# Kernel tuning notes

Hardware: AMD Instinct MI355X
Metric: run time of the kernel (lower is better)

## Reference

```python
import jax, jax.numpy as jnp
import numpy as np

IDIM = 1024
ODIM = 1024
NHEADS = 16
B, S = 4, 1024


def setup_inputs() -> dict:
    key = jax.random.key(0)
    k1, k2, k3, k4, k5, k6 = jax.random.split(key, 6)
    m_feats = jax.random.normal(k1, (B, S, IDIM), dtype=jnp.float32)
    mask = jax.random.randint(k2, (B, S), 0, 2, dtype=jnp.int32)
    # torch Linear weights stored pre-transposed: y = x @ W + b
    W_c = jax.random.normal(k3, (IDIM, 2 * ODIM), dtype=jnp.float32) * 0.02
    b_c = jnp.zeros((2 * ODIM,), dtype=jnp.float32)
    W_v = jax.random.normal(k4, (IDIM, ODIM), dtype=jnp.float32) * 0.02
    b_v = jnp.zeros((ODIM,), dtype=jnp.float32)
    return {"m_feats": m_feats, "mask": mask, "W_c": W_c, "b_c": b_c, "W_v": W_v, "b_v": b_v}


def reference(m_feats, mask, W_c, b_c, W_v, b_v):
    # dp = 0.0 -> dropout is identity (eval-mode equivalence)
    Bn, Sn, _ = m_feats.shape
    odim = W_v.shape[1]
    dh = odim // NHEADS
    m_k = m_feats @ W_v + b_v            # v_lin  -> keys   [B,S,odim]
    m_trans = m_feats @ W_c + b_c        # c_lin  -> [B,S,2*odim]
    m_q = m_trans[..., :odim]            # queries
    m_v = m_trans[..., odim:]            # values
    mk = m_k.reshape(Bn, Sn, NHEADS, dh)
    mq = m_q.reshape(Bn, Sn, NHEADS, dh)
    mv = m_v.reshape(Bn, Sn, NHEADS, dh)
    # original: scores = K @ Q^T / sqrt(dh); softmax over the Q (last) axis
    scores = jnp.einsum('bihd,bjhd->bhij', mk, mq) / jnp.sqrt(jnp.float32(dh))
    maskf = mask.astype(jnp.float32)
    scores = jnp.where(maskf[:, None, None, :] == 0.0, jnp.float32(-1e9), scores)
    w = jax.nn.softmax(scores, axis=-1)               # [B,H,S,S]
    r = jnp.einsum('bhij,bjhd->bihd', w, mv).reshape(Bn, Sn, odim)
    updated_m = m_feats + r
    return updated_m, w
```

## Files before the change

kernel.cpp:

```cpp
#include <hip/hip_runtime.h>
#include <cstddef>

typedef short short8 __attribute__((ext_vector_type(8)));
typedef float f32x4 __attribute__((ext_vector_type(4)));

#define SS 1024
#define NH 16
#define DH 64
#define NB 4

static __device__ __forceinline__ unsigned short f2bf(float f) {
    union { float f; unsigned int i; } x; x.f = f;
    unsigned int r = x.i + 0x7FFFu + ((x.i >> 16) & 1u);
    return (unsigned short)(r >> 16);
}
static __device__ __forceinline__ float bf2f(unsigned short u) {
    union { unsigned int i; float f; } x; x.i = ((unsigned int)u) << 16;
    return x.f;
}

static __device__ __forceinline__ void g2l16(const void* g, void* l) {
    __builtin_amdgcn_global_load_lds(
        (const __attribute__((address_space(1))) unsigned int*)g,
        (__attribute__((address_space(3))) unsigned int*)l, 16, 0, 0);
}

__global__ __launch_bounds__(256) void cast_mf(const float* __restrict__ in,
                                               unsigned short* __restrict__ out) {
    size_t i = ((size_t)blockIdx.x * 256 + threadIdx.x) * 4;
    float4 v = *(const float4*)(in + i);
    short4 o;
    o.x = (short)f2bf(v.x); o.y = (short)f2bf(v.y);
    o.z = (short)f2bf(v.z); o.w = (short)f2bf(v.w);
    *(short4*)(out + i) = o;
}

__global__ __launch_bounds__(256) void transpose_w(const float* __restrict__ Wv,
                                                   const float* __restrict__ Wc,
                                                   unsigned short* __restrict__ WT) {
    __shared__ float tile[32][33];
    int n0 = blockIdx.x * 32, k0 = blockIdx.y * 32;
    int t = threadIdx.x;
    int kr = t >> 3, nc = (t & 7) * 4;
    const float* src; int ld; int nn = n0 + nc;
    if (n0 < 1024) { src = Wv; ld = 1024; } else { src = Wc; ld = 2048; nn -= 1024; }
    float4 v = *(const float4*)(src + (size_t)(k0 + kr) * ld + nn);
    tile[kr][nc + 0] = v.x; tile[kr][nc + 1] = v.y;
    tile[kr][nc + 2] = v.z; tile[kr][nc + 3] = v.w;
    __syncthreads();
    int nr = t >> 3, kc = (t & 7) * 4;
    short4 o;
    o.x = (short)f2bf(tile[kc + 0][nr]); o.y = (short)f2bf(tile[kc + 1][nr]);
    o.z = (short)f2bf(tile[kc + 2][nr]); o.w = (short)f2bf(tile[kc + 3][nr]);
    *(short4*)(WT + (size_t)(n0 + nr) * 1024 + k0 + kc) = o;
}

__global__ __launch_bounds__(256) void gemm_kqv(const unsigned short* __restrict__ A,
                                                const unsigned short* __restrict__ BT,
                                                const float* __restrict__ bv,
                                                const float* __restrict__ bc,
                                                unsigned short* __restrict__ kq,
                                                unsigned short* __restrict__ mv) {
    __shared__ __align__(16) unsigned short As[128 * 32];
    __shared__ __align__(16) unsigned short Bs[128 * 32];
    int m0 = blockIdx.y * 128;
    int n0 = blockIdx.x * 128;
    int tid = threadIdx.x, lane = tid & 63, wv = tid >> 6;
    int wm = wv >> 1, wn = wv & 1;
    int lq = lane & 15, quad = lane >> 4;

    f32x4 zero = {0.f, 0.f, 0.f, 0.f};
    f32x4 acc[4][4];
#pragma unroll
    for (int i = 0; i < 4; ++i)
#pragma unroll
        for (int j = 0; j < 4; ++j) acc[i][j] = zero;

    int r0 = tid >> 2, s0 = tid & 3;
    int c0 = s0 ^ ((r0 >> 1) & 3);
    int r1 = (tid + 256) >> 2, s1 = tid & 3;
    int c1 = s1 ^ ((r1 >> 1) & 3);

    const unsigned short* Abase0 = A + (size_t)(m0 + r0) * 1024 + c0 * 8;
    const unsigned short* Abase1 = A + (size_t)(m0 + r1) * 1024 + c1 * 8;
    const unsigned short* Bbase0 = BT + (size_t)(n0 + r0) * 1024 + c0 * 8;
    const unsigned short* Bbase1 = BT + (size_t)(n0 + r1) * 1024 + c1 * 8;

    for (int kt = 0; kt < 1024; kt += 32) {
        __syncthreads();
        g2l16(Abase0 + kt, As + tid * 8);
        g2l16(Abase1 + kt, As + (tid + 256) * 8);
        g2l16(Bbase0 + kt, Bs + tid * 8);
        g2l16(Bbase1 + kt, Bs + (tid + 256) * 8);
        __syncthreads();

        short8 af[4], bfr[4];
#pragma unroll
        for (int i = 0; i < 4; ++i) {
            int Ra = wm * 64 + i * 16 + lq;
            af[i] = *(const short8*)(As + Ra * 32 + (quad ^ ((Ra >> 1) & 3)) * 8);
            int Rb = wn * 64 + i * 16 + lq;
            bfr[i] = *(const short8*)(Bs + Rb * 32 + (quad ^ ((Rb >> 1) & 3)) * 8);
        }
#pragma unroll
        for (int mi = 0; mi < 4; ++mi)
#pragma unroll
            for (int ni = 0; ni < 4; ++ni)
                acc[mi][ni] = __builtin_amdgcn_mfma_f32_16x16x32_bf16(af[mi], bfr[ni], acc[mi][ni], 0, 0, 0);
    }

#pragma unroll
    for (int mi = 0; mi < 4; ++mi) {
#pragma unroll
        for (int ni = 0; ni < 4; ++ni) {
            int colg = n0 + wn * 64 + ni * 16 + lq;
            float bias = (colg < 1024) ? bv[colg] : bc[colg - 1024];
            if (colg < 2048) {
#pragma unroll
                for (int r = 0; r < 4; ++r) {
                    int rowg = m0 + wm * 64 + mi * 16 + quad * 4 + r;
                    kq[(size_t)rowg * 2048 + colg] = f2bf(acc[mi][ni][r] + bias);
                }
            } else {
                int c = colg - 2048;
#pragma unroll
                for (int r = 0; r < 4; ++r) {
                    int rowg = m0 + wm * 64 + mi * 16 + quad * 4 + r;
                    mv[(size_t)rowg * 1024 + c] = f2bf(acc[mi][ni][r] + bias);
                }
            }
        }
    }
}

__global__ __launch_bounds__(256) void transpose_mv(const unsigned short* __restrict__ mv,
                                                    unsigned short* __restrict__ mvT) {
    __shared__ __align__(16) unsigned short tile[64 * 72];
    int bh = blockIdx.y, j0 = blockIdx.x * 64;
    int b = bh >> 4, h = bh & 15;
    int t = threadIdx.x;

    int j = t >> 2;
#pragma unroll
    for (int it = 0; it < 2; ++it) {
        int c = (t & 3) + it * 4;
        short8 v = *(const short8*)(mv + (size_t)(b * SS + j0 + j) * 1024 + h * 64 + c * 8);
        *(short8*)(tile + j * 72 + c * 8) = v;
    }
    __syncthreads();

    int d = t >> 2, jc = t & 3;
    unsigned short* dst = mvT + ((size_t)bh * DH + d) * 1024 + j0 + jc * 16;
#pragma unroll
    for (int half = 0; half < 2; ++half) {
        short8 o;
#pragma unroll
        for (int k = 0; k < 8; ++k) o[k] = (short)tile[(jc * 16 + half * 8 + k) * 72 + d];
        *(short8*)(dst + half * 8) = o;
    }
}

__global__ __launch_bounds__(256, 4) void attn_kernel(const unsigned short* __restrict__ kq,
                                                      const unsigned short* __restrict__ mvT,
                                                      const int* __restrict__ mask,
                                                      const float* __restrict__ m_feats,
                                                      float* __restrict__ out0,
                                                      float* __restrict__ out1) {
    __shared__ __align__(16) unsigned short mk_s[16 * 72];
    __shared__ __align__(16) unsigned short s_exp[16 * 1032];
    __shared__ __align__(16) int mask_s[1024];
    __shared__ float wsum[4][16];
    __shared__ float inv_s[16];

    int tid = threadIdx.x;
    int lane = tid & 63, wv = tid >> 6;
    int lq = lane & 15, quad = lane >> 4;

    int blk = ((int)blockIdx.x & 7) * 512 + ((int)blockIdx.x >> 3);
    int it = blk & 63;
    int bh = blk >> 6;
    int h = bh & (NH - 1), b = bh >> 4;
    int i0 = it * 16;

    {
        int4 mv4 = *(const int4*)(mask + (size_t)b * SS + tid * 4);
        *(int4*)(mask_s + tid * 4) = mv4;
    }

    if (tid < 128) {
        int row = tid >> 3, ch = tid & 7;
        int4 v = *(const int4*)(kq + (size_t)(b * SS + i0 + row) * 2048 + h * 64 + ch * 8);
        *(int4*)(mk_s + row * 72 + ch * 8) = v;
    }
    __syncthreads();

    short8 a0 = *(const short8*)(mk_s + lq * 72 + 0 * 32 + quad * 8);
    short8 a1 = *(const short8*)(mk_s + lq * 72 + 1 * 32 + quad * 8);

    float sums[4] = {0.f, 0.f, 0.f, 0.f};
    const float SC = 0.18033688011112042f;
    const unsigned short* mqb = kq + (size_t)b * SS * 2048 + 1024 + h * 64 + quad * 8;

    short8 qb[2][4][2];
    int qm[2][4];

#define QLOAD(p, s)                                                          \
    {                                                                        \
        int jb_ = (s) * 256 + wv * 64;                                       \
        _Pragma("unroll") for (int js = 0; js < 4; ++js) {                   \
            int jg_ = jb_ + js * 16 + lq;                                    \
            size_t ro_ = (size_t)jg_ * 2048;                                 \
            qb[p][js][0] = *(const short8*)(mqb + ro_);                      \
            qb[p][js][1] = *(const short8*)(mqb + ro_ + 32);                 \
            qm[p][js] = mask_s[jg_];                                         \
        }                                                                    \
    }

#define QCOMP(p, s)                                                          \
    {                                                                        \
        int jb_ = (s) * 256 + wv * 64;                                       \
        _Pragma("unroll") for (int js = 0; js < 4; ++js) {                   \
            f32x4 acc = {0.f, 0.f, 0.f, 0.f};                                \
            acc = __builtin_amdgcn_mfma_f32_16x16x32_bf16(a0, qb[p][js][0], acc, 0, 0, 0); \
            acc = __builtin_amdgcn_mfma_f32_16x16x32_bf16(a1, qb[p][js][1], acc, 0, 0, 0); \
            int jc_ = jb_ + js * 16 + lq;                                    \
            _Pragma("unroll") for (int r = 0; r < 4; ++r) {                  \
                float e = qm[p][js] ? __builtin_amdgcn_exp2f(acc[r] * SC) : 0.f; \
                sums[r] += e;                                                \
                s_exp[(quad * 4 + r) * 1032 + jc_] = f2bf(e);                \
            }                                                                \
        }                                                                    \
    }

    QLOAD(0, 0);
    QLOAD(1, 1); QCOMP(0, 0);
    QLOAD(0, 2); QCOMP(1, 1);
    QLOAD(1, 3); QCOMP(0, 2);
    QCOMP(1, 3);
#undef QLOAD
#undef QCOMP

#pragma unroll
    for (int r = 0; r < 4; ++r) {
        float s = sums[r];
        s += __shfl_xor(s, 1); s += __shfl_xor(s, 2);
        s += __shfl_xor(s, 4); s += __shfl_xor(s, 8);
        if (lq == 0) wsum[wv][quad * 4 + r] = s;
    }
    __syncthreads();
    if (tid < 16) {
        float s = wsum[0][tid] + wsum[1][tid] + wsum[2][tid] + wsum[3][tid];
        inv_s[tid] = 1.0f / s;
    }
    __syncthreads();

    f32x4 racc = {0.f, 0.f, 0.f, 0.f};
    const unsigned short* mvb = mvT + ((size_t)bh * DH + wv * 16 + lq) * 1024 + quad * 8;
    short8 vbuf[2][4];

#define VLOAD(p, ko)                                                         \
    {                                                                        \
        _Pragma("unroll") for (int k2 = 0; k2 < 4; ++k2)                     \
            vbuf[p][k2] = *(const short8*)(mvb + ((ko) * 4 + k2) * 32);      \
    }

#define VCOMP(p, ko)                                                         \
    {                                                                        \
        _Pragma("unroll") for (int k2 = 0; k2 < 4; ++k2) {                   \
            short8 ae = *(const short8*)(s_exp + lq * 1032 + ((ko) * 4 + k2) * 32 + quad * 8); \
            racc = __builtin_amdgcn_mfma_f32_16x16x32_bf16(ae, vbuf[p][k2], racc, 0, 0, 0); \
        }                                                                    \
    }

    VLOAD(0, 0);
    VLOAD(1, 1); VCOMP(0, 0);
    VLOAD(0, 2); VCOMP(1, 1);
    VLOAD(1, 3); VCOMP(0, 2);
    VLOAD(0, 4); VCOMP(1, 3);
    VLOAD(1, 5); VCOMP(0, 4);
    VLOAD(0, 6); VCOMP(1, 5);
    VLOAD(1, 7); VCOMP(0, 6);
    VCOMP(1, 7);
#undef VLOAD
#undef VCOMP

#pragma unroll
    for (int r = 0; r < 4; ++r) {
        int row = quad * 4 + r;
        size_t o = (size_t)(b * SS + i0 + row) * 1024 + h * 64 + wv * 16 + lq;
        __builtin_nontemporal_store(m_feats[o] + racc[r] * inv_s[row], out0 + o);
    }

    size_t wbase = ((size_t)bh * SS + i0) * SS;
#pragma unroll 4
    for (int r = 0; r < 16; ++r) {
        float iv = inv_s[r];
        short4 ev = *(const short4*)(s_exp + r * 1032 + tid * 4);
        f32x4 wo;
        wo[0] = bf2f((unsigned short)ev.x) * iv;
        wo[1] = bf2f((unsigned short)ev.y) * iv;
        wo[2] = bf2f((unsigned short)ev.z) * iv;
        wo[3] = bf2f((unsigned short)ev.w) * iv;
        __builtin_nontemporal_store(wo, (f32x4*)(out1 + wbase + (size_t)r * SS + tid * 4));
    }
}

extern "C" void kernel_launch(void* const* d_in, const int* in_sizes, int n_in,
                              void* d_out, int out_size, void* d_ws, size_t ws_size,
                              hipStream_t stream) {
    const float* m_feats = (const float*)d_in[0];
    const int*   mask    = (const int*)d_in[1];
    const float* W_c     = (const float*)d_in[2];
    const float* b_c     = (const float*)d_in[3];
    const float* W_v     = (const float*)d_in[4];
    const float* b_v     = (const float*)d_in[5];

    float* out0 = (float*)d_out;
    float* out1 = out0 + (size_t)NB * SS * 1024;

    unsigned short* mf_bf = (unsigned short*)d_ws;
    unsigned short* WT    = mf_bf + (size_t)4096 * 1024;
    unsigned short* kq    = WT + (size_t)3072 * 1024;
    unsigned short* mv    = kq + (size_t)4096 * 2048;
    unsigned short* mvT   = mf_bf;

    cast_mf<<<dim3(4096), dim3(256), 0, stream>>>(m_feats, mf_bf);
    transpose_w<<<dim3(96, 32), dim3(256), 0, stream>>>(W_v, W_c, WT);
    gemm_kqv<<<dim3(24, 32), dim3(256), 0, stream>>>(mf_bf, WT, b_v, b_c, kq, mv);
    transpose_mv<<<dim3(16, 64), dim3(256), 0, stream>>>(mv, mvT);
    attn_kernel<<<dim3(4096), dim3(256), 0, stream>>>(kq, mvT, mask, m_feats, out0, out1);
}
```

Before: 435.6 us.

## Fuse prep kernels, write transposed V from GEMM, interleave attention output stores

Merges the cast and weight-transpose kernels into one launch. The GEMM now writes V directly in transposed layout, which removes the separate transpose kernel but turns those epilogue stores into strided scalar writes. The GEMM block order is remapped so tiles group by XCD. In the attention kernel, the mask is read straight from global memory instead of being staged in shared memory, and the m_feats residual loads and the mk tile load are overlapped with the first Q loads. The attention weight stores are also interleaved with the PV MFMAs using a deeper 4-stage V buffer, which raises register pressure.

```diff
diff --git a/kernel.cpp b/kernel.cpp
--- a/kernel.cpp
+++ b/kernel.cpp
@@ -25,22 +25,25 @@
         (__attribute__((address_space(3))) unsigned int*)l, 16, 0, 0);
 }
 
-__global__ __launch_bounds__(256) void cast_mf(const float* __restrict__ in,
-                                               unsigned short* __restrict__ out) {
-    size_t i = ((size_t)blockIdx.x * 256 + threadIdx.x) * 4;
-    float4 v = *(const float4*)(in + i);
-    short4 o;
-    o.x = (short)f2bf(v.x); o.y = (short)f2bf(v.y);
-    o.z = (short)f2bf(v.z); o.w = (short)f2bf(v.w);
-    *(short4*)(out + i) = o;
-}
-
-__global__ __launch_bounds__(256) void transpose_w(const float* __restrict__ Wv,
-                                                   const float* __restrict__ Wc,
-                                                   unsigned short* __restrict__ WT) {
+__global__ __launch_bounds__(256) void prep(const float* __restrict__ mf,
+                                            unsigned short* __restrict__ mfb,
+                                            const float* __restrict__ Wv,
+                                            const float* __restrict__ Wc,
+                                            unsigned short* __restrict__ WT) {
     __shared__ float tile[32][33];
-    int n0 = blockIdx.x * 32, k0 = blockIdx.y * 32;
+    int bx = blockIdx.x;
     int t = threadIdx.x;
+    if (bx < 4096) {
+        size_t i = ((size_t)bx * 256 + t) * 4;
+        float4 v = *(const float4*)(mf + i);
+        short4 o;
+        o.x = (short)f2bf(v.x); o.y = (short)f2bf(v.y);
+        o.z = (short)f2bf(v.z); o.w = (short)f2bf(v.w);
+        *(short4*)(mfb + i) = o;
+        return;
+    }
+    bx -= 4096;
+    int n0 = (bx % 96) * 32, k0 = (bx / 96) * 32;
     int kr = t >> 3, nc = (t & 7) * 4;
     const float* src; int ld; int nn = n0 + nc;
     if (n0 < 1024) { src = Wv; ld = 1024; } else { src = Wc; ld = 2048; nn -= 1024; }
@@ -60,11 +63,16 @@
                                                 const float* __restrict__ bv,
                                                 const float* __restrict__ bc,
                                                 unsigned short* __restrict__ kq,
-                                                unsigned short* __restrict__ mv) {
+                                                unsigned short* __restrict__ mvT) {
     __shared__ __align__(16) unsigned short As[128 * 32];
     __shared__ __align__(16) unsigned short Bs[128 * 32];
-    int m0 = blockIdx.y * 128;
-    int n0 = blockIdx.x * 128;
+    int lin = blockIdx.y * 24 + blockIdx.x;
+    int xcd = lin & 7, idx = lin >> 3;
+    int cx = xcd & 1, cy = xcd >> 1;
+    int xi = idx % 12, yi = idx / 12;
+    int n0 = (cx * 12 + xi) * 128;
+    int m0 = (cy * 8 + yi) * 128;
+
     int tid = threadIdx.x, lane = tid & 63, wv = tid >> 6;
     int wm = wv >> 1, wn = wv & 1;
     int lq = lane & 15, quad = lane >> 4;
@@ -123,40 +131,16 @@
                 }
             } else {
                 int c = colg - 2048;
+                int hh = c >> 6, dd = c & 63;
 #pragma unroll
                 for (int r = 0; r < 4; ++r) {
                     int rowg = m0 + wm * 64 + mi * 16 + quad * 4 + r;
-                    mv[(size_t)rowg * 1024 + c] = f2bf(acc[mi][ni][r] + bias);
+                    int bb = rowg >> 10, jj = rowg & 1023;
+                    mvT[((size_t)(bb * NH + hh) * DH + dd) * 1024 + jj] =
+                        f2bf(acc[mi][ni][r] + bias);
                 }
             }
         }
-    }
-}
-
-__global__ __launch_bounds__(256) void transpose_mv(const unsigned short* __restrict__ mv,
-                                                    unsigned short* __restrict__ mvT) {
-    __shared__ __align__(16) unsigned short tile[64 * 72];
-    int bh = blockIdx.y, j0 = blockIdx.x * 64;
-    int b = bh >> 4, h = bh & 15;
-    int t = threadIdx.x;
-
-    int j = t >> 2;
-#pragma unroll
-    for (int it = 0; it < 2; ++it) {
-        int c = (t & 3) + it * 4;
-        short8 v = *(const short8*)(mv + (size_t)(b * SS + j0 + j) * 1024 + h * 64 + c * 8);
-        *(short8*)(tile + j * 72 + c * 8) = v;
-    }
-    __syncthreads();
-
-    int d = t >> 2, jc = t & 3;
-    unsigned short* dst = mvT + ((size_t)bh * DH + d) * 1024 + j0 + jc * 16;
-#pragma unroll
-    for (int half = 0; half < 2; ++half) {
-        short8 o;
-#pragma unroll
-        for (int k = 0; k < 8; ++k) o[k] = (short)tile[(jc * 16 + half * 8 + k) * 72 + d];
-        *(short8*)(dst + half * 8) = o;
     }
 }
 
@@ -168,7 +152,6 @@
                                                       float* __restrict__ out1) {
     __shared__ __align__(16) unsigned short mk_s[16 * 72];
     __shared__ __align__(16) unsigned short s_exp[16 * 1032];
-    __shared__ __align__(16) int mask_s[1024];
     __shared__ float wsum[4][16];
     __shared__ float inv_s[16];
 
@@ -182,27 +165,13 @@
     int h = bh & (NH - 1), b = bh >> 4;
     int i0 = it * 16;
 
-    {
-        int4 mv4 = *(const int4*)(mask + (size_t)b * SS + tid * 4);
-        *(int4*)(mask_s + tid * 4) = mv4;
-    }
-
-    if (tid < 128) {
-        int row = tid >> 3, ch = tid & 7;
-        int4 v = *(const int4*)(kq + (size_t)(b * SS + i0 + row) * 2048 + h * 64 + ch * 8);
-        *(int4*)(mk_s + row * 72 + ch * 8) = v;
-    }
-    __syncthreads();
-
-    short8 a0 = *(const short8*)(mk_s + lq * 72 + 0 * 32 + quad * 8);
-    short8 a1 = *(const short8*)(mk_s + lq * 72 + 1 * 32 + quad * 8);
-
-    float sums[4] = {0.f, 0.f, 0.f, 0.f};
     const float SC = 0.18033688011112042f;
     const unsigned short* mqb = kq + (size_t)b * SS * 2048 + 1024 + h * 64 + quad * 8;
+    const int* maskb = mask + (size_t)b * SS;
 
     short8 qb[2][4][2];
     int qm[2][4];
+    float sums[4] = {0.f, 0.f, 0.f, 0.f};
 
 #define QLOAD(p, s)                                                          \
     {                                                                        \
@@ -212,7 +181,7 @@
             size_t ro_ = (size_t)jg_ * 2048;                                 \
             qb[p][js][0] = *(const short8*)(mqb + ro_);                      \
             qb[p][js][1] = *(const short8*)(mqb + ro_ + 32);                 \
-            qm[p][js] = mask_s[jg_];                                         \
+            qm[p][js] = maskb[jg_];                                          \
         }                                                                    \
     }
 
@@ -233,9 +202,28 @@
     }
 
     QLOAD(0, 0);
-    QLOAD(1, 1); QCOMP(0, 0);
-    QLOAD(0, 2); QCOMP(1, 1);
-    QLOAD(1, 3); QCOMP(0, 2);
+
+    float mf4[4];
+#pragma unroll
+    for (int r = 0; r < 4; ++r) {
+        size_t o = (size_t)(b * SS + i0 + quad * 4 + r) * 1024 + h * 64 + wv * 16 + lq;
+        mf4[r] = m_feats[o];
+    }
+
+    if (tid < 128) {
+        int row = tid >> 3, ch = tid & 7;
+        int4 v = *(const int4*)(kq + (size_t)(b * SS + i0 + row) * 2048 + h * 64 + ch * 8);
+        *(int4*)(mk_s + row * 72 + ch * 8) = v;
+    }
+    QLOAD(1, 1);
+    __syncthreads();
+
+    short8 a0 = *(const short8*)(mk_s + lq * 72 + 0 * 32 + quad * 8);
+    short8 a1 = *(const short8*)(mk_s + lq * 72 + 1 * 32 + quad * 8);
+
+    QCOMP(0, 0); QLOAD(0, 2);
+    QCOMP(1, 1); QLOAD(1, 3);
+    QCOMP(0, 2);
     QCOMP(1, 3);
 #undef QLOAD
 #undef QCOMP
@@ -256,7 +244,8 @@
 
     f32x4 racc = {0.f, 0.f, 0.f, 0.f};
     const unsigned short* mvb = mvT + ((size_t)bh * DH + wv * 16 + lq) * 1024 + quad * 8;
-    short8 vbuf[2][4];
+    size_t wbase = ((size_t)bh * SS + i0) * SS;
+    short8 vbuf[4][4];
 
 #define VLOAD(p, ko)                                                         \
     {                                                                        \
@@ -272,36 +261,36 @@
         }                                                                    \
     }
 
-    VLOAD(0, 0);
-    VLOAD(1, 1); VCOMP(0, 0);
-    VLOAD(0, 2); VCOMP(1, 1);
-    VLOAD(1, 3); VCOMP(0, 2);
-    VLOAD(0, 4); VCOMP(1, 3);
-    VLOAD(1, 5); VCOMP(0, 4);
-    VLOAD(0, 6); VCOMP(1, 5);
-    VLOAD(1, 7); VCOMP(0, 6);
-    VCOMP(1, 7);
+#define WOUT(r)                                                              \
+    {                                                                        \
+        float iv = inv_s[r];                                                 \
+        short4 ev = *(const short4*)(s_exp + (r) * 1032 + tid * 4);          \
+        f32x4 wo;                                                            \
+        wo[0] = bf2f((unsigned short)ev.x) * iv;                             \
+        wo[1] = bf2f((unsigned short)ev.y) * iv;                             \
+        wo[2] = bf2f((unsigned short)ev.z) * iv;                             \
+        wo[3] = bf2f((unsigned short)ev.w) * iv;                             \
+        __builtin_nontemporal_store(wo, (f32x4*)(out1 + wbase + (size_t)(r) * SS + tid * 4)); \
+    }
+
+    VLOAD(0, 0); VLOAD(1, 1); VLOAD(2, 2); VLOAD(3, 3);
+    VCOMP(0, 0); VLOAD(0, 4); WOUT(0);  WOUT(1);
+    VCOMP(1, 1); VLOAD(1, 5); WOUT(2);  WOUT(3);
+    VCOMP(2, 2); VLOAD(2, 6); WOUT(4);  WOUT(5);
+    VCOMP(3, 3); VLOAD(3, 7); WOUT(6);  WOUT(7);
+    VCOMP(0, 4); WOUT(8);  WOUT(9);
+    VCOMP(1, 5); WOUT(10); WOUT(11);
+    VCOMP(2, 6); WOUT(12); WOUT(13);
+    VCOMP(3, 7); WOUT(14); WOUT(15);
 #undef VLOAD
 #undef VCOMP
+#undef WOUT
 
 #pragma unroll
     for (int r = 0; r < 4; ++r) {
         int row = quad * 4 + r;
         size_t o = (size_t)(b * SS + i0 + row) * 1024 + h * 64 + wv * 16 + lq;
-        __builtin_nontemporal_store(m_feats[o] + racc[r] * inv_s[row], out0 + o);
-    }
-
-    size_t wbase = ((size_t)bh * SS + i0) * SS;
-#pragma unroll 4
-    for (int r = 0; r < 16; ++r) {
-        float iv = inv_s[r];
-        short4 ev = *(const short4*)(s_exp + r * 1032 + tid * 4);
-        f32x4 wo;
-        wo[0] = bf2f((unsigned short)ev.x) * iv;
-        wo[1] = bf2f((unsigned short)ev.y) * iv;
-        wo[2] = bf2f((unsigned short)ev.z) * iv;
-        wo[3] = bf2f((unsigned short)ev.w) * iv;
-        __builtin_nontemporal_store(wo, (f32x4*)(out1 + wbase + (size_t)r * SS + tid * 4));
+        __builtin_nontemporal_store(mf4[r] + racc[r] * inv_s[row], out0 + o);
     }
 }
 
@@ -321,12 +310,9 @@
     unsigned short* mf_bf = (unsigned short*)d_ws;
     unsigned short* WT    = mf_bf + (size_t)4096 * 1024;
     unsigned short* kq    = WT + (size_t)3072 * 1024;
-    unsigned short* mv    = kq + (size_t)4096 * 2048;
-    unsigned short* mvT   = mf_bf;
-
-    cast_mf<<<dim3(4096), dim3(256), 0, stream>>>(m_feats, mf_bf);
-    transpose_w<<<dim3(96, 32), dim3(256), 0, stream>>>(W_v, W_c, WT);
-    gemm_kqv<<<dim3(24, 32), dim3(256), 0, stream>>>(mf_bf, WT, b_v, b_c, kq, mv);
-    transpose_mv<<<dim3(16, 64), dim3(256), 0, stream>>>(mv, mvT);
+    unsigned short* mvT   = kq + (size_t)4096 * 2048;
+
+    prep<<<dim3(7168), dim3(256), 0, stream>>>(m_feats, mf_bf, W_v, W_c, WT);
+    gemm_kqv<<<dim3(24, 32), dim3(256), 0, stream>>>(mf_bf, WT, b_v, b_c, kq, mvT);
     attn_kernel<<<dim3(4096), dim3(256), 0, stream>>>(kq, mvT, mask, m_feats, out0, out1);
 }
```

New measurement: 433.2 us. No clear change (-0.6%).
